# Optimization experiments

Hardware: AMD Instinct MI355X
Metric: run time of the kernel (lower is better)

The kernel has to match this reference:

```python
import jax, jax.numpy as jnp
import numpy as np

N, E, G = 10000, 40000, 128
ATOM, EDGE, STATE = 32, 32, 16
D = ATOM + STATE  # 48, dynamic per-edge weight is DxD
STEPS = 2


def setup_inputs() -> dict:
    key = jax.random.key(0)
    ks = jax.random.split(key, 24)
    pair = jax.random.randint(ks[0], (E, 2), 0, N, dtype=jnp.int32)
    pair = pair[jnp.argsort(pair[:, 0])]  # tf.math.segment_sum needs sorted ids
    agi = jnp.sort(jax.random.randint(ks[1], (N,), 0, G, dtype=jnp.int32))
    bgi = jnp.sort(jax.random.randint(ks[2], (E,), 0, G, dtype=jnp.int32))
    s = 0.05
    return {
        "atom_features": jax.random.normal(ks[3], (N, ATOM), jnp.float32),
        "edges_features": jax.random.normal(ks[4], (E, EDGE), jnp.float32),
        "state_attrs": jax.random.normal(ks[5], (G, STATE), jnp.float32),
        "pair_indices": pair,
        "atom_graph_indices": agi,
        "bond_graph_indices": bgi,
        "kernel": jax.random.normal(ks[6], (EDGE, D * D), jnp.float32) * s,
        "bias": jnp.zeros((D * D,), jnp.float32),
        "We": jax.random.normal(ks[7], (2 * ATOM + STATE + EDGE, 3 * EDGE), jnp.float32) * s,
        "Ue": jax.random.normal(ks[8], (EDGE, 3 * EDGE), jnp.float32) * s,
        "be_in": jnp.zeros((3 * EDGE,), jnp.float32),
        "be_rec": jnp.zeros((3 * EDGE,), jnp.float32),
        "Wn": jax.random.normal(ks[9], (D, 3 * ATOM), jnp.float32) * s,
        "Un": jax.random.normal(ks[10], (ATOM, 3 * ATOM), jnp.float32) * s,
        "bn_in": jnp.zeros((3 * ATOM,), jnp.float32),
        "bn_rec": jnp.zeros((3 * ATOM,), jnp.float32),
        "Ws": jax.random.normal(ks[11], (ATOM + EDGE + STATE, 3 * STATE), jnp.float32) * s,
        "Us": jax.random.normal(ks[12], (STATE, 3 * STATE), jnp.float32) * s,
        "bs_in": jnp.zeros((3 * STATE,), jnp.float32),
        "bs_rec": jnp.zeros((3 * STATE,), jnp.float32),
    }


def _gru(x, h, W, U, b_in, b_rec):
    # Keras GRUCell, reset_after=True; gate order [z, r, h]
    xz, xr, xh = jnp.split(x @ W + b_in, 3, axis=-1)
    hz, hr, hh = jnp.split(h @ U + b_rec, 3, axis=-1)
    z = jax.nn.sigmoid(xz + hz)
    r = jax.nn.sigmoid(xr + hr)
    hcand = jnp.tanh(xh + r * hh)
    return z * h + (1.0 - z) * hcand


def reference(atom_features, edges_features, state_attrs, pair_indices,
              atom_graph_indices, bond_graph_indices, kernel, bias,
              We, Ue, be_in, be_rec, Wn, Un, bn_in, bn_rec,
              Ws, Us, bs_in, bs_rec):
    a, e, s = atom_features, edges_features, state_attrs
    n_nodes = a.shape[0]
    n_graphs = s.shape[0]
    src, dst = pair_indices[:, 0], pair_indices[:, 1]
    for _ in range(STEPS):
        # concat_edges + edge GRU update
        e_cat = jnp.concatenate([a[src], a[dst], s[bond_graph_indices], e], axis=-1)
        e = _gru(e_cat, e, We, Ue, be_in, be_rec)
        # aggregate_nodes: per-edge dynamic DxD weight, matvec on dst feats, scatter-add to src
        amc = jnp.concatenate([a, s[atom_graph_indices]], axis=-1)  # (N, D)
        w = (e @ kernel + bias).reshape(-1, D, D)                    # (E, D, D)
        t = jnp.einsum('eij,ej->ei', w, amc[dst])                    # (E, D)
        agg = jax.ops.segment_sum(t, src, num_segments=n_nodes)      # (N, D)
        a = _gru(agg, a, Wn, Un, bn_in, bn_rec)
        # concat_states + state GRU update
        a_sum = jax.ops.segment_sum(a, atom_graph_indices, num_segments=n_graphs)
        e_sum = jax.ops.segment_sum(e, bond_graph_indices, num_segments=n_graphs)
        s = _gru(jnp.concatenate([a_sum, e_sum, s], axis=-1), s, Ws, Us, bs_in, bs_rec)
    return (a, e, s)
```

## Files before the change

### kernel.cpp

```cpp
#include <hip/hip_runtime.h>

#define N_ATOMS 10000
#define N_EDGES 40000
#define N_GRAPH 128

typedef unsigned short ushort_t;
typedef __attribute__((ext_vector_type(8))) short bf16x8;
typedef __attribute__((ext_vector_type(4))) float f32x4;

__device__ __forceinline__ ushort_t f2bf(float f) {
    unsigned int u = __float_as_uint(f);
    unsigned int r = (u + 0x7fffu + ((u >> 16) & 1u)) >> 16;
    return (ushort_t)r;
}
__device__ __forceinline__ float bf2f(ushort_t u) { return __uint_as_float(((unsigned int)u) << 16); }
__device__ __forceinline__ float bflo(unsigned int u) { return __uint_as_float(u << 16); }
__device__ __forceinline__ float bfhi(unsigned int u) { return __uint_as_float(u & 0xffff0000u); }

__global__ void trans_k(const float* __restrict__ We, const float* __restrict__ Ue,
                        const float* __restrict__ Wn, const float* __restrict__ Un,
                        const float* __restrict__ kernelw,
                        float* __restrict__ wta, float* __restrict__ wts,
                        float* __restrict__ wtee, float* __restrict__ wtn,
                        float* __restrict__ wtun, ushort_t* __restrict__ kb)
{
    int idx = blockIdx.x * 256 + threadIdx.x;
    if (idx < 6144) {
        int c = idx / 32, k = idx % 32;
        int col = c % 96;
        int srck = (c < 96) ? k : 32 + k;
        wta[idx] = We[srck * 96 + col];
    } else if (idx < 7680) {
        int j = idx - 6144; int c = j / 16, k = j % 16;
        wts[j] = We[(64 + k) * 96 + c];
    } else if (idx < 13824) {
        int j = idx - 7680; int c = j / 32, k = j % 32;
        wtee[j] = (c < 96) ? We[(80 + k) * 96 + c] : Ue[k * 96 + (c - 96)];
    } else if (idx < 18432) {
        int j = idx - 13824; int c = j / 48, k = j % 48;
        wtn[j] = Wn[k * 96 + c];
    } else if (idx < 21504) {
        int j = idx - 18432; int c = j / 32, k = j % 32;
        wtun[j] = Un[k * 96 + c];
    } else {
        int j = idx - 21504;
        kb[j] = f2bf(kernelw[j]);
    }
}

__global__ __launch_bounds__(192) void pa_k(const float* __restrict__ a,
                                            const float* __restrict__ wta,
                                            float* __restrict__ PA)
{
    __shared__ float as_[16][32];
    int t = threadIdx.x;
    int n0 = blockIdx.x * 16;
    if (t < 128) reinterpret_cast<float4*>(&as_[0][0])[t] =
        reinterpret_cast<const float4*>(a + (size_t)n0 * 32)[t];
    __syncthreads();

    float w[32];
    const float4* wp4 = reinterpret_cast<const float4*>(wta + t * 32);
    #pragma unroll
    for (int q = 0; q < 8; ++q) {
        float4 v = wp4[q];
        w[4*q] = v.x; w[4*q+1] = v.y; w[4*q+2] = v.z; w[4*q+3] = v.w;
    }
    #pragma unroll
    for (int i = 0; i < 16; ++i) {
        float sres = 0.f;
        #pragma unroll
        for (int k = 0; k < 32; ++k) sres += as_[i][k] * w[k];
        PA[(size_t)(n0 + i) * 192 + t] = sres;
    }
}

__global__ __launch_bounds__(96) void ps_k(const float* __restrict__ s,
                                           const float* __restrict__ wts,
                                           const float* __restrict__ be_in,
                                           float* __restrict__ PS)
{
    __shared__ float ss[16][16];
    int t = threadIdx.x;
    int g0 = blockIdx.x * 16;
    if (t < 64) reinterpret_cast<float4*>(&ss[0][0])[t] =
        reinterpret_cast<const float4*>(s + (size_t)g0 * 16)[t];
    __syncthreads();

    float w[16];
    const float4* wp4 = reinterpret_cast<const float4*>(wts + t * 16);
    #pragma unroll
    for (int q = 0; q < 4; ++q) {
        float4 v = wp4[q];
        w[4*q] = v.x; w[4*q+1] = v.y; w[4*q+2] = v.z; w[4*q+3] = v.w;
    }
    float b = be_in[t];
    #pragma unroll
    for (int i = 0; i < 16; ++i) {
        float sres = b;
        #pragma unroll
        for (int k = 0; k < 16; ++k) sres += ss[i][k] * w[k];
        PS[(size_t)(g0 + i) * 96 + t] = sres;
    }
}

__global__ __launch_bounds__(192) void edge_fused_k(const float* __restrict__ e_in,
                                                    const float* __restrict__ wtee,
                                                    const float* __restrict__ be_rec,
                                                    const float* __restrict__ PA,
                                                    const float* __restrict__ PS,
                                                    const int* __restrict__ pair,
                                                    const int* __restrict__ bgi,
                                                    float* __restrict__ e_out,
                                                    float* __restrict__ esum)
{
    __shared__ float es[16][32];
    __shared__ float S[16][192];
    __shared__ int garr[16];
    int t = threadIdx.x;
    int e0b = blockIdx.x * 16;

    if (t < 128) reinterpret_cast<float4*>(&es[0][0])[t] =
        reinterpret_cast<const float4*>(e_in + (size_t)e0b * 32)[t];
    if (t >= 128 && t < 144) garr[t - 128] = bgi[e0b + (t - 128)];
    __syncthreads();

    float w[32];
    const float4* wp4 = reinterpret_cast<const float4*>(wtee + t * 32);
    #pragma unroll
    for (int q = 0; q < 8; ++q) {
        float4 v = wp4[q];
        w[4*q] = v.x; w[4*q+1] = v.y; w[4*q+2] = v.z; w[4*q+3] = v.w;
    }
    float b = (t >= 96) ? be_rec[t - 96] : 0.f;
    #pragma unroll 4
    for (int i = 0; i < 16; ++i) {
        float sres = b;
        #pragma unroll
        for (int k = 0; k < 32; ++k) sres += es[i][k] * w[k];
        S[i][t] = sres;
    }
    __syncthreads();

    for (int idx = t; idx < 512; idx += 192) {
        int le = idx >> 5, cc = idx & 31;
        int eid = e0b + le;
        int src = pair[2 * eid], dst = pair[2 * eid + 1];
        const float* pas = PA + (size_t)src * 192;
        const float* pad = PA + (size_t)dst * 192 + 96;
        const float* ps  = PS + (size_t)garr[le] * 96;
        float xz = pas[cc]      + pad[cc]      + ps[cc]      + S[le][cc];
        float xr = pas[32 + cc] + pad[32 + cc] + ps[32 + cc] + S[le][32 + cc];
        float xh = pas[64 + cc] + pad[64 + cc] + ps[64 + cc] + S[le][64 + cc];
        float hz = S[le][96 + cc], hr = S[le][128 + cc], hh = S[le][160 + cc];
        float h  = es[le][cc];
        float z  = 1.f / (1.f + expf(-(xz + hz)));
        float r  = 1.f / (1.f + expf(-(xr + hr)));
        float hc = tanhf(xh + r * hh);
        float val = z * h + (1.f - z) * hc;
        e_out[(size_t)eid * 32 + cc] = val;
        es[le][cc] = val;
    }
    __syncthreads();

    if (t < 32) {
        int cc = t;
        int gprev = garr[0];
        float run = 0.f;
        #pragma unroll 4
        for (int le = 0; le < 16; ++le) {
            int gcur = garr[le];
            if (gcur != gprev) {
                atomicAdd(&esum[gprev * 32 + cc], run);
                run = 0.f; gprev = gcur;
            }
            run += es[le][cc];
        }
        atomicAdd(&esum[gprev * 32 + cc], run);
    }
}

__global__ __launch_bounds__(256) void y_mfma_k(const ushort_t* __restrict__ kb,
                                                const float* __restrict__ bias,
                                                const float* __restrict__ a,
                                                const float* __restrict__ s,
                                                const int* __restrict__ agi,
                                                ushort_t* __restrict__ Yb,
                                                float* __restrict__ Bn)
{
    __shared__ ushort_t amcs[32][64];
    int t = threadIdx.x;
    int n0 = blockIdx.x * 32;

    for (int idx = t; idx < 32 * 64; idx += 256) {
        int row = idx >> 6, j = idx & 63;
        int n = n0 + row;
        float v = 0.f;
        if (n < N_ATOMS) {
            if (j < 32)      v = a[(size_t)n * 32 + j];
            else if (j < 48) v = s[agi[n] * 16 + (j - 32)];
        }
        amcs[row][j] = f2bf(v);
    }
    __syncthreads();

    int lane = t & 63;
    int wv = t >> 6;
    int cl = lane & 15;
    int g  = lane >> 4;

    bf16x8 zero8 = {0, 0, 0, 0, 0, 0, 0, 0};

    bf16x8 A[2][2];
    #pragma unroll
    for (int mt = 0; mt < 2; ++mt) {
        #pragma unroll
        for (int kh = 0; kh < 2; ++kh) {
            A[mt][kh] = *reinterpret_cast<const bf16x8*>(&amcs[mt * 16 + cl][kh * 32 + g * 8]);
        }
    }

    for (int nt = wv; nt < 96; nt += 4) {
        int c = nt * 16 + cl;
        int kk = c & 31, ii = c >> 5;
        const ushort_t* kbase = kb + (size_t)kk * 2304 + ii * 48;
        bf16x8 B0 = *reinterpret_cast<const bf16x8*>(kbase + g * 8);
        bf16x8 B1 = (g < 2) ? *reinterpret_cast<const bf16x8*>(kbase + 32 + g * 8) : zero8;
        #pragma unroll
        for (int mt = 0; mt < 2; ++mt) {
            f32x4 acc = {0.f, 0.f, 0.f, 0.f};
            acc = __builtin_amdgcn_mfma_f32_16x16x32_bf16(A[mt][0], B0, acc, 0, 0, 0);
            acc = __builtin_amdgcn_mfma_f32_16x16x32_bf16(A[mt][1], B1, acc, 0, 0, 0);
            #pragma unroll
            for (int r = 0; r < 4; ++r) {
                int n = n0 + mt * 16 + g * 4 + r;
                if (n < N_ATOMS) Yb[(size_t)n * 1536 + c] = f2bf(acc[r]);
            }
        }
    }

    for (int idx = t; idx < 32 * 48; idx += 256) {
        int row = idx / 48, i = idx % 48;
        int n = n0 + row;
        if (n >= N_ATOMS) continue;
        const float* bb = bias + i * 48;
        float accv = 0.f;
        #pragma unroll
        for (int j = 0; j < 48; ++j) accv += bb[j] * bf2f(amcs[row][j]);
        Bn[(size_t)n * 48 + i] = accv;
    }
}

__global__ __launch_bounds__(256) void edge_msg_k(const float* __restrict__ e_new,
                                                  const int* __restrict__ pair,
                                                  const ushort_t* __restrict__ Yb,
                                                  const float* __restrict__ Bn,
                                                  float* __restrict__ agg)
{
    int t = threadIdx.x;
    int lane = t & 63;
    int eid = blockIdx.x * 4 + (t >> 6);
    if (lane >= 48) return;
    int src = pair[2 * eid], dst = pair[2 * eid + 1];

    float ev[32];
    const float4* ep = reinterpret_cast<const float4*>(e_new + (size_t)eid * 32);
    #pragma unroll
    for (int q = 0; q < 8; ++q) {
        float4 v = ep[q];
        ev[4*q] = v.x; ev[4*q+1] = v.y; ev[4*q+2] = v.z; ev[4*q+3] = v.w;
    }

    const uint4* yp = reinterpret_cast<const uint4*>(Yb + (size_t)dst * 1536 + lane * 32);
    float acc = Bn[dst * 48 + lane];
    #pragma unroll
    for (int q = 0; q < 4; ++q) {
        uint4 v = yp[q];
        int k = q * 8;
        acc += bflo(v.x) * ev[k]     + bfhi(v.x) * ev[k + 1]
             + bflo(v.y) * ev[k + 2] + bfhi(v.y) * ev[k + 3]
             + bflo(v.z) * ev[k + 4] + bfhi(v.z) * ev[k + 5]
             + bflo(v.w) * ev[k + 6] + bfhi(v.w) * ev[k + 7];
    }
    atomicAdd(&agg[src * 48 + lane], acc);
}

__global__ __launch_bounds__(192) void node_fused_k(const float* __restrict__ agg,
                                                    const float* __restrict__ a_in,
                                                    const float* __restrict__ wtn,
                                                    const float* __restrict__ wtun,
                                                    const float* __restrict__ bn_in,
                                                    const float* __restrict__ bn_rec,
                                                    const int* __restrict__ agi,
                                                    float* __restrict__ a_out,
                                                    float* __restrict__ asum)
{
    __shared__ float xs[16][48];
    __shared__ float hs[16][32];
    __shared__ float S[16][192];
    __shared__ int garr[16];
    int t = threadIdx.x;
    int n0 = blockIdx.x * 16;

    reinterpret_cast<float4*>(&xs[0][0])[t] =
        reinterpret_cast<const float4*>(agg + (size_t)n0 * 48)[t];
    if (t < 128) reinterpret_cast<float4*>(&hs[0][0])[t] =
        reinterpret_cast<const float4*>(a_in + (size_t)n0 * 32)[t];
    if (t >= 128 && t < 144) garr[t - 128] = agi[n0 + (t - 128)];
    __syncthreads();

    if (t < 96) {
        float w[48];
        const float4* wp4 = reinterpret_cast<const float4*>(wtn + t * 48);
        #pragma unroll
        for (int q = 0; q < 12; ++q) {
            float4 v = wp4[q];
            w[4*q] = v.x; w[4*q+1] = v.y; w[4*q+2] = v.z; w[4*q+3] = v.w;
        }
        float b = bn_in[t];
        #pragma unroll 4
        for (int i = 0; i < 16; ++i) {
            float sres = b;
            #pragma unroll
            for (int k = 0; k < 48; ++k) sres += xs[i][k] * w[k];
            S[i][t] = sres;
        }
    } else {
        float w[32];
        const float4* wp4 = reinterpret_cast<const float4*>(wtun + (t - 96) * 32);
        #pragma unroll
        for (int q = 0; q < 8; ++q) {
            float4 v = wp4[q];
            w[4*q] = v.x; w[4*q+1] = v.y; w[4*q+2] = v.z; w[4*q+3] = v.w;
        }
        float b = bn_rec[t - 96];
        #pragma unroll 4
        for (int i = 0; i < 16; ++i) {
            float sres = b;
            #pragma unroll
            for (int k = 0; k < 32; ++k) sres += hs[i][k] * w[k];
            S[i][t] = sres;
        }
    }
    __syncthreads();

    for (int idx = t; idx < 512; idx += 192) {
        int le = idx >> 5, cc = idx & 31;
        int n = n0 + le;
        float z  = 1.f / (1.f + expf(-(S[le][cc] + S[le][96 + cc])));
        float r  = 1.f / (1.f + expf(-(S[le][32 + cc] + S[le][128 + cc])));
        float hc = tanhf(S[le][64 + cc] + r * S[le][160 + cc]);
        float h  = hs[le][cc];
        float val = z * h + (1.f - z) * hc;
        a_out[(size_t)n * 32 + cc] = val;
        hs[le][cc] = val;
    }
    __syncthreads();

    if (t < 32) {
        int cc = t;
        int gprev = garr[0];
        float run = 0.f;
        #pragma unroll 4
        for (int le = 0; le < 16; ++le) {
            int gcur = garr[le];
            if (gcur != gprev) {
                atomicAdd(&asum[gprev * 32 + cc], run);
                run = 0.f; gprev = gcur;
            }
            run += hs[le][cc];
        }
        atomicAdd(&asum[gprev * 32 + cc], run);
    }
}

__global__ void state_gru_k(const float* __restrict__ asum, const float* __restrict__ esum,
                            const float* __restrict__ s_in,
                            const float* __restrict__ Ws, const float* __restrict__ Us,
                            const float* __restrict__ bs_in, const float* __restrict__ bs_rec,
                            float* __restrict__ s_out)
{
    __shared__ float xs[80];
    __shared__ float hsv[16];
    __shared__ float S[48];
    __shared__ float Uh[16];
    int g = blockIdx.x;
    int t = threadIdx.x;
    if (t < 80) {
        float v;
        if (t < 32)      v = asum[g * 32 + t];
        else if (t < 64) v = esum[g * 32 + (t - 32)];
        else             v = s_in[g * 16 + (t - 64)];
        xs[t] = v;
        if (t >= 64) hsv[t - 64] = v;
    }
    __syncthreads();
    if (t < 48) {
        float gacc = bs_in[t];
        #pragma unroll
        for (int k = 0; k < 80; ++k) gacc += xs[k] * Ws[k * 48 + t];
        float u = bs_rec[t];
        #pragma unroll
        for (int k = 0; k < 16; ++k) u += hsv[k] * Us[k * 48 + t];
        if (t < 32) { S[t] = gacc + u; }
        else        { S[t] = gacc; Uh[t - 32] = u; }
    }
    __syncthreads();
    if (t < 16) {
        float z  = 1.f / (1.f + expf(-S[t]));
        float r  = 1.f / (1.f + expf(-S[16 + t]));
        float hc = tanhf(S[32 + t] + r * Uh[t]);
        s_out[g * 16 + t] = z * hsv[t] + (1.f - z) * hc;
    }
}

extern "C" void kernel_launch(void* const* d_in, const int* in_sizes, int n_in,
                              void* d_out, int out_size, void* d_ws, size_t ws_size,
                              hipStream_t stream)
{
    const float* a0      = (const float*)d_in[0];
    const float* e0      = (const float*)d_in[1];
    const float* s0      = (const float*)d_in[2];
    const int*   pair    = (const int*)d_in[3];
    const int*   agi     = (const int*)d_in[4];
    const int*   bgi     = (const int*)d_in[5];
    const float* kernelw = (const float*)d_in[6];
    const float* bias    = (const float*)d_in[7];
    const float* We      = (const float*)d_in[8];
    const float* Ue      = (const float*)d_in[9];
    const float* be_in   = (const float*)d_in[10];
    const float* be_rec  = (const float*)d_in[11];
    const float* Wn      = (const float*)d_in[12];
    const float* Un      = (const float*)d_in[13];
    const float* bn_in   = (const float*)d_in[14];
    const float* bn_rec  = (const float*)d_in[15];
    const float* Ws      = (const float*)d_in[16];
    const float* Us      = (const float*)d_in[17];
    const float* bs_in   = (const float*)d_in[18];
    const float* bs_rec  = (const float*)d_in[19];

    float* out_a = (float*)d_out;
    float* out_e = out_a + N_ATOMS * 32;
    float* out_s = out_e + (size_t)N_EDGES * 32;

    char* wp = (char*)d_ws;
    auto alloc = [&](size_t nf) { float* p = (float*)wp; wp += nf * sizeof(float); return p; };
    float* aW   = alloc((size_t)N_ATOMS * 32);
    float* eW   = alloc((size_t)N_EDGES * 32);
    float* sW   = alloc((size_t)N_GRAPH * 16);
    ushort_t* Yb = (ushort_t*)alloc((size_t)N_ATOMS * 1536 / 2);
    float* Bn   = alloc((size_t)N_ATOMS * 48);
    float* agg  = alloc((size_t)N_ATOMS * 48);
    float* asum = alloc((size_t)N_GRAPH * 32);
    float* esum = alloc((size_t)N_GRAPH * 32);
    float* PA   = alloc((size_t)N_ATOMS * 192);
    float* PS   = alloc((size_t)N_GRAPH * 96);
    float* wta  = alloc(6144);
    float* wts  = alloc(1536);
    float* wtee = alloc(6144);
    float* wtn  = alloc(4608);
    float* wtun = alloc(3072);
    ushort_t* kb = (ushort_t*)alloc(36864);
    size_t zero_bytes = ((size_t)N_ATOMS * 48 + 2 * N_GRAPH * 32) * sizeof(float);

    trans_k<<<372, 256, 0, stream>>>(We, Ue, Wn, Un, kernelw,
                                     wta, wts, wtee, wtn, wtun, kb);

    const float* a_in = a0;
    const float* e_in = e0;
    const float* s_in = s0;

    for (int step = 0; step < 2; ++step) {
        float* a_o = (step == 0) ? aW : out_a;
        float* e_o = (step == 0) ? eW : out_e;
        float* s_o = (step == 0) ? sW : out_s;

        hipMemsetAsync(agg, 0, zero_bytes, stream);
        pa_k<<<N_ATOMS / 16, 192, 0, stream>>>(a_in, wta, PA);
        ps_k<<<N_GRAPH / 16, 96, 0, stream>>>(s_in, wts, be_in, PS);
        edge_fused_k<<<N_EDGES / 16, 192, 0, stream>>>(e_in, wtee, be_rec, PA, PS,
                                                       pair, bgi, e_o, esum);
        y_mfma_k<<<(N_ATOMS + 31) / 32, 256, 0, stream>>>(kb, bias, a_in, s_in, agi, Yb, Bn);
        edge_msg_k<<<N_EDGES / 4, 256, 0, stream>>>(e_o, pair, Yb, Bn, agg);
        node_fused_k<<<N_ATOMS / 16, 192, 0, stream>>>(agg, a_in, wtn, wtun,
                                                       bn_in, bn_rec, agi, a_o, asum);
        state_gru_k<<<N_GRAPH, 128, 0, stream>>>(asum, esum, s_in, Ws, Us, bs_in, bs_rec, s_o);

        a_in = a_o; e_in = e_o; s_in = s_o;
    }
}
```

Before: 311.3 us.

## Replace atomic edge scatter with CSR row-pointer node-centric aggregation

Builds a CSR row pointer over the source-sorted edge list with a binary-search kernel. The per-edge message kernel becomes a per-node kernel that loops over that node's edges and writes agg directly. This removes the float atomics and most of the per-step memset of agg. In exchange, per-node edge counts vary, so load is uneven, and each wave now processes its edges one after another.

Result: slower. 323.2 us (+3.8%).

```diff
diff --git a/kernel.cpp b/kernel.cpp
--- a/kernel.cpp
+++ b/kernel.cpp
@@ -48,6 +48,18 @@
     }
 }
 
+__global__ void rowptr_k(const int* __restrict__ pair, int* __restrict__ rowptr)
+{
+    int n = blockIdx.x * 256 + threadIdx.x;
+    if (n > N_ATOMS) return;
+    int lo = 0, hi = N_EDGES;
+    while (lo < hi) {
+        int mid = (lo + hi) >> 1;
+        if (pair[2 * mid] < n) lo = mid + 1; else hi = mid;
+    }
+    rowptr[n] = lo;
+}
+
 __global__ __launch_bounds__(192) void pa_k(const float* __restrict__ a,
                                             const float* __restrict__ wta,
                                             float* __restrict__ PA)
@@ -251,38 +263,43 @@
     }
 }
 
-__global__ __launch_bounds__(256) void edge_msg_k(const float* __restrict__ e_new,
+__global__ __launch_bounds__(256) void node_agg_k(const float* __restrict__ e_new,
                                                   const int* __restrict__ pair,
                                                   const ushort_t* __restrict__ Yb,
                                                   const float* __restrict__ Bn,
+                                                  const int* __restrict__ rowptr,
                                                   float* __restrict__ agg)
 {
     int t = threadIdx.x;
     int lane = t & 63;
-    int eid = blockIdx.x * 4 + (t >> 6);
-    if (lane >= 48) return;
-    int src = pair[2 * eid], dst = pair[2 * eid + 1];
-
-    float ev[32];
-    const float4* ep = reinterpret_cast<const float4*>(e_new + (size_t)eid * 32);
-    #pragma unroll
-    for (int q = 0; q < 8; ++q) {
-        float4 v = ep[q];
-        ev[4*q] = v.x; ev[4*q+1] = v.y; ev[4*q+2] = v.z; ev[4*q+3] = v.w;
-    }
-
-    const uint4* yp = reinterpret_cast<const uint4*>(Yb + (size_t)dst * 1536 + lane * 32);
-    float acc = Bn[dst * 48 + lane];
-    #pragma unroll
-    for (int q = 0; q < 4; ++q) {
-        uint4 v = yp[q];
-        int k = q * 8;
-        acc += bflo(v.x) * ev[k]     + bfhi(v.x) * ev[k + 1]
-             + bflo(v.y) * ev[k + 2] + bfhi(v.y) * ev[k + 3]
-             + bflo(v.z) * ev[k + 4] + bfhi(v.z) * ev[k + 5]
-             + bflo(v.w) * ev[k + 6] + bfhi(v.w) * ev[k + 7];
-    }
-    atomicAdd(&agg[src * 48 + lane], acc);
+    int n = blockIdx.x * 4 + (t >> 6);
+    if (n >= N_ATOMS || lane >= 48) return;
+
+    int e0 = rowptr[n], e1 = rowptr[n + 1];
+    float acc = 0.f;
+    for (int eid = e0; eid < e1; ++eid) {
+        int dst = pair[2 * eid + 1];
+        float ev[32];
+        const float4* ep = reinterpret_cast<const float4*>(e_new + (size_t)eid * 32);
+        #pragma unroll
+        for (int q = 0; q < 8; ++q) {
+            float4 v = ep[q];
+            ev[4*q] = v.x; ev[4*q+1] = v.y; ev[4*q+2] = v.z; ev[4*q+3] = v.w;
+        }
+        const uint4* yp = reinterpret_cast<const uint4*>(Yb + (size_t)dst * 1536 + lane * 32);
+        float sres = Bn[dst * 48 + lane];
+        #pragma unroll
+        for (int q = 0; q < 4; ++q) {
+            uint4 v = yp[q];
+            int k = q * 8;
+            sres += bflo(v.x) * ev[k]     + bfhi(v.x) * ev[k + 1]
+                  + bflo(v.y) * ev[k + 2] + bfhi(v.y) * ev[k + 3]
+                  + bflo(v.z) * ev[k + 4] + bfhi(v.z) * ev[k + 5]
+                  + bflo(v.w) * ev[k + 6] + bfhi(v.w) * ev[k + 7];
+        }
+        acc += sres;
+    }
+    agg[(size_t)n * 48 + lane] = acc;
 }
 
 __global__ __launch_bounds__(192) void node_fused_k(const float* __restrict__ agg,
@@ -461,10 +478,12 @@
     float* wtn  = alloc(4608);
     float* wtun = alloc(3072);
     ushort_t* kb = (ushort_t*)alloc(36864);
-    size_t zero_bytes = ((size_t)N_ATOMS * 48 + 2 * N_GRAPH * 32) * sizeof(float);
+    int* rowptr = (int*)alloc(N_ATOMS + 1);
+    size_t zero_bytes = (size_t)2 * N_GRAPH * 32 * sizeof(float);
 
     trans_k<<<372, 256, 0, stream>>>(We, Ue, Wn, Un, kernelw,
                                      wta, wts, wtee, wtn, wtun, kb);
+    rowptr_k<<<41, 256, 0, stream>>>(pair, rowptr);
 
     const float* a_in = a0;
     const float* e_in = e0;
@@ -475,13 +494,13 @@
         float* e_o = (step == 0) ? eW : out_e;
         float* s_o = (step == 0) ? sW : out_s;
 
-        hipMemsetAsync(agg, 0, zero_bytes, stream);
+        hipMemsetAsync(asum, 0, zero_bytes, stream);
         pa_k<<<N_ATOMS / 16, 192, 0, stream>>>(a_in, wta, PA);
         ps_k<<<N_GRAPH / 16, 96, 0, stream>>>(s_in, wts, be_in, PS);
         edge_fused_k<<<N_EDGES / 16, 192, 0, stream>>>(e_in, wtee, be_rec, PA, PS,
                                                        pair, bgi, e_o, esum);
         y_mfma_k<<<(N_ATOMS + 31) / 32, 256, 0, stream>>>(kb, bias, a_in, s_in, agi, Yb, Bn);
-        edge_msg_k<<<N_EDGES / 4, 256, 0, stream>>>(e_o, pair, Yb, Bn, agg);
+        node_agg_k<<<(N_ATOMS + 3) / 4, 256, 0, stream>>>(e_o, pair, Yb, Bn, rowptr, agg);
         node_fused_k<<<N_ATOMS / 16, 192, 0, stream>>>(agg, a_in, wtn, wtun,
                                                        bn_in, bn_rec, agi, a_o, asum);
         state_gru_k<<<N_GRAPH, 128, 0, stream>>>(asum, esum, s_in, Ws, Us, bs_in, bs_rec, s_o);
```
